# Performance work log

Measured on AMD Instinct MI355X. Metric: run time of the kernel, lower is better.

Reference implementation:

```python
import jax, jax.numpy as jnp
import numpy as np


def setup_inputs() -> dict:
    key = jax.random.key(0)
    ks = jax.random.split(key, 8)
    B, H, W, C = 4, 64, 64, 64
    Cf = C // 8
    x = jax.random.normal(ks[0], (B, H, W, C), dtype=jnp.float32)
    # 1x1 conv kernels stored as [C_in, C_out] (kernel_size=1)
    w_f = jax.random.normal(ks[1], (C, Cf), dtype=jnp.float32) * 0.05
    b_f = jax.random.normal(ks[2], (Cf,), dtype=jnp.float32) * 0.05
    w_g = jax.random.normal(ks[3], (C, Cf), dtype=jnp.float32) * 0.05
    b_g = jax.random.normal(ks[4], (Cf,), dtype=jnp.float32) * 0.05
    w_h = jax.random.normal(ks[5], (C, C), dtype=jnp.float32) * 0.05
    b_h = jax.random.normal(ks[6], (C,), dtype=jnp.float32) * 0.05
    gamma = jax.random.normal(ks[7], (1,), dtype=jnp.float32) * 0.1
    return {"x": x, "w_f": w_f, "b_f": b_f, "w_g": w_g, "b_g": b_g,
            "w_h": w_h, "b_h": b_h, "gamma": gamma}


def reference(x, w_f, b_f, w_g, b_g, w_h, b_h, gamma):
    B, H, W, C = x.shape
    N = H * W
    xf = x.reshape(B, N, C)  # 1x1 conv == per-pixel linear
    f = xf @ w_f + b_f       # [B, N, C/8]
    g = xf @ w_g + b_g       # [B, N, C/8]
    h = xf @ w_h + b_h       # [B, N, C]
    # attention_map[b, i, j] = <g_i, f_j>, softmax over last axis
    scores = jnp.einsum('bic,bjc->bij', g, f)  # [B, N, N]
    attn = jax.nn.softmax(scores, axis=-1)
    out = jnp.einsum('bij,bjc->bic', attn, h)  # [B, N, C]
    out = out.reshape(B, H, W, C)
    return gamma * out + x
```

## Files before the change

### kernel.cpp

```cpp
#include <hip/hip_runtime.h>
#include <hip/hip_bf16.h>

typedef __bf16 bf16;
typedef __bf16 bf16x8 __attribute__((ext_vector_type(8)));
typedef __bf16 bf16x4 __attribute__((ext_vector_type(4)));
typedef float floatx4 __attribute__((ext_vector_type(4)));

typedef int  aint  __attribute__((may_alias));
typedef long along __attribute__((may_alias));

#define NPIX 4096
#define BATCH 4
#define LOG2E 1.4426950408889634f
#define HT_BATCH 262144

__device__ inline bf16x8 zero8() {
    bf16x8 v;
    #pragma unroll
    for (int i = 0; i < 8; ++i) v[i] = (bf16)0.0f;
    return v;
}

__global__ __launch_bounds__(256) void proj_kernel(
    const float* __restrict__ x,
    const float* __restrict__ w_f, const float* __restrict__ b_f,
    const float* __restrict__ w_g, const float* __restrict__ b_g,
    const float* __restrict__ w_h, const float* __restrict__ b_h,
    bf16* __restrict__ fq, bf16* __restrict__ gq, unsigned char* __restrict__ hT)
{
    __shared__ bf16 xs[64 * 72];
    __shared__ bf16 wt[80 * 72];
    __shared__ float bs[80];
    const int tid = threadIdx.x;
    const int p0 = blockIdx.x * 64;

    {
        const float4* xg = (const float4*)(x + (long)p0 * 64);
        #pragma unroll
        for (int it = 0; it < 4; ++it) {
            int i4 = tid + it * 256;
            float4 v = xg[i4];
            int row = i4 >> 4, c4 = (i4 & 15) * 4;
            bf16x4 pk;
            pk[0] = (bf16)v.x; pk[1] = (bf16)v.y; pk[2] = (bf16)v.z; pk[3] = (bf16)v.w;
            *(bf16x4*)(&xs[row * 72 + c4]) = pk;
        }
    }
    for (int idx = tid; idx < 512; idx += 256) {
        int c = idx >> 3, n = idx & 7;
        wt[n * 72 + c]       = (bf16)w_f[idx];
        wt[(8 + n) * 72 + c] = (bf16)w_g[idx];
    }
    #pragma unroll
    for (int it = 0; it < 16; ++it) {
        int idx = tid + it * 256;
        int c = idx >> 6, n = idx & 63;
        wt[(16 + n) * 72 + c] = (bf16)w_h[idx];
    }
    if (tid < 80)
        bs[tid] = (tid < 8) ? b_f[tid] : (tid < 16) ? b_g[tid - 8] : b_h[tid - 16];
    __syncthreads();

    const int wv = tid >> 6, lane = tid & 63;
    const int quad = lane >> 4, l15 = lane & 15;
    const int b = blockIdx.x >> 6;
    const int n0pix = (p0 & (NPIX - 1)) + wv * 16 + quad * 4;

    bf16x8 a0 = *(const bf16x8*)(&xs[(wv * 16 + l15) * 72 + quad * 8]);
    bf16x8 a1 = *(const bf16x8*)(&xs[(wv * 16 + l15) * 72 + 32 + quad * 8]);

    #pragma unroll
    for (int nt = 0; nt < 5; ++nt) {
        float bias = bs[nt * 16 + l15];
        floatx4 acc = {bias, bias, bias, bias};
        bf16x8 b0 = *(const bf16x8*)(&wt[(nt * 16 + l15) * 72 + quad * 8]);
        bf16x8 b1 = *(const bf16x8*)(&wt[(nt * 16 + l15) * 72 + 32 + quad * 8]);
        acc = __builtin_amdgcn_mfma_f32_16x16x32_bf16(a0, b0, acc, 0, 0, 0);
        acc = __builtin_amdgcn_mfma_f32_16x16x32_bf16(a1, b1, acc, 0, 0, 0);
        if (nt == 0) {
            #pragma unroll
            for (int r = 0; r < 4; ++r) {
                long P = (long)p0 + wv * 16 + quad * 4 + r;
                if (l15 < 8) fq[P * 8 + l15] = (bf16)acc[r];
                else         gq[P * 8 + (l15 - 8)] = (bf16)(acc[r] * LOG2E);
            }
        } else {
            int c = nt * 16 + l15 - 16;
            int pk = __builtin_amdgcn_cvt_pk_fp8_f32(acc[0], acc[1], 0, false);
            pk     = __builtin_amdgcn_cvt_pk_fp8_f32(acc[2], acc[3], pk, true);
            *(aint*)(hT + (long)b * HT_BATCH + (n0pix >> 5) * 2048
                     + c * 32 + (n0pix & 31)) = pk;
        }
    }
}

__global__ __launch_bounds__(256, 4) void attn_kernel(
    const bf16* __restrict__ fq, const bf16* __restrict__ gq,
    const unsigned char* __restrict__ hT, const float* __restrict__ x,
    const float* __restrict__ gamma_p, float* __restrict__ out)
{
    __shared__ float red[4 * 32 * 68];
    const int tid  = threadIdx.x;
    const int wv   = tid >> 6, lane = tid & 63;
    const int quad = lane >> 4, l15 = lane & 15;
    const int jq   = wv;
    const int xcd = blockIdx.x & 7;
    const int b   = xcd >> 1;
    const int it  = ((blockIdx.x >> 3) & 63) | ((xcd & 1) << 6);
    const long rowbase = (long)b * NPIX + it * 32;
    const int jbase = jq * 1024;

    bf16x8 gfragA = zero8(), gfragB = zero8();
    if (lane < 16) {
        gfragA = *(const bf16x8*)(gq + (rowbase + lane) * 8);
        gfragB = *(const bf16x8*)(gq + (rowbase + 16 + lane) * 8);
    }

    const bf16* Fb = fq + ((long)b * NPIX + jbase) * 8;
    const unsigned char* Hb = hT + (long)b * HT_BATCH + (jbase >> 5) * 2048
                            + (l15 * 32 + quad * 8);

    floatx4 acc[8];
    #pragma unroll
    for (int k = 0; k < 8; ++k) acc[k] = (floatx4){0.f, 0.f, 0.f, 0.f};
    float denA = 0.f, denB = 0.f;

    const int idx_lo = (((quad & 1) * 2) * 16 + l15) * 4;
    const int idx_hi = idx_lo + 64;
    const bool sel_b = (quad >> 1) != 0;

    for (int t = 0; t < 8; ++t) {
        bf16x8 af[8];
        #pragma unroll
        for (int j8 = 0; j8 < 8; ++j8) {
            af[j8] = zero8();
            if (lane < 16)
                af[j8] = *(const bf16x8*)(Fb + (t * 128 + j8 * 16 + l15) * 8);
        }
        along bfr[16];
        #pragma unroll
        for (int ks = 0; ks < 4; ++ks)
            #pragma unroll
            for (int nt = 0; nt < 4; ++nt)
                bfr[ks * 4 + nt] = *(const along*)(Hb + (t * 4 + ks) * 2048 + nt * 512);

        int pkA[8], pkB[8];
        #pragma unroll
        for (int j8 = 0; j8 < 8; ++j8) {
            floatx4 sA = __builtin_amdgcn_mfma_f32_16x16x32_bf16(
                af[j8], gfragA, (floatx4){0.f, 0.f, 0.f, 0.f}, 0, 0, 0);
            floatx4 sB = __builtin_amdgcn_mfma_f32_16x16x32_bf16(
                af[j8], gfragB, (floatx4){0.f, 0.f, 0.f, 0.f}, 0, 0, 0);
            float a0 = __builtin_amdgcn_exp2f(sA[0]);
            float a1 = __builtin_amdgcn_exp2f(sA[1]);
            float a2 = __builtin_amdgcn_exp2f(sA[2]);
            float a3 = __builtin_amdgcn_exp2f(sA[3]);
            float b0 = __builtin_amdgcn_exp2f(sB[0]);
            float b1 = __builtin_amdgcn_exp2f(sB[1]);
            float b2 = __builtin_amdgcn_exp2f(sB[2]);
            float b3 = __builtin_amdgcn_exp2f(sB[3]);
            denA += (a0 + a1) + (a2 + a3);
            denB += (b0 + b1) + (b2 + b3);
            int pa = __builtin_amdgcn_cvt_pk_fp8_f32(a0, a1, 0, false);
            pkA[j8] = __builtin_amdgcn_cvt_pk_fp8_f32(a2, a3, pa, true);
            int pb = __builtin_amdgcn_cvt_pk_fp8_f32(b0, b1, 0, false);
            pkB[j8] = __builtin_amdgcn_cvt_pk_fp8_f32(b2, b3, pb, true);
        }
        #pragma unroll
        for (int ks = 0; ks < 4; ++ks) {
            int loA0 = __builtin_amdgcn_ds_bpermute(idx_lo, pkA[2 * ks]);
            int loA1 = __builtin_amdgcn_ds_bpermute(idx_lo, pkA[2 * ks + 1]);
            int hiA0 = __builtin_amdgcn_ds_bpermute(idx_hi, pkA[2 * ks]);
            int hiA1 = __builtin_amdgcn_ds_bpermute(idx_hi, pkA[2 * ks + 1]);
            unsigned loA = (unsigned)(sel_b ? loA1 : loA0);
            unsigned hiA = (unsigned)(sel_b ? hiA1 : hiA0);
            along pfA = (along)(((unsigned long)hiA << 32) | loA);
            int loB0 = __builtin_amdgcn_ds_bpermute(idx_lo, pkB[2 * ks]);
            int loB1 = __builtin_amdgcn_ds_bpermute(idx_lo, pkB[2 * ks + 1]);
            int hiB0 = __builtin_amdgcn_ds_bpermute(idx_hi, pkB[2 * ks]);
            int hiB1 = __builtin_amdgcn_ds_bpermute(idx_hi, pkB[2 * ks + 1]);
            unsigned loB = (unsigned)(sel_b ? loB1 : loB0);
            unsigned hiB = (unsigned)(sel_b ? hiB1 : hiB0);
            along pfB = (along)(((unsigned long)hiB << 32) | loB);
            #pragma unroll
            for (int nt = 0; nt < 4; ++nt) {
                acc[nt]     = __builtin_amdgcn_mfma_f32_16x16x32_fp8_fp8(
                    pfA, bfr[ks * 4 + nt], acc[nt], 0, 0, 0);
                acc[4 + nt] = __builtin_amdgcn_mfma_f32_16x16x32_fp8_fp8(
                    pfB, bfr[ks * 4 + nt], acc[4 + nt], 0, 0, 0);
            }
        }
    }

    denA += __shfl_xor(denA, 16);  denA += __shfl_xor(denA, 32);
    denB += __shfl_xor(denB, 16);  denB += __shfl_xor(denB, 32);

    {
        const int rbA = (jq * 32 + quad * 4) * 68;
        const int rbB = (jq * 32 + 16 + quad * 4) * 68;
        #pragma unroll
        for (int nt = 0; nt < 4; ++nt)
            #pragma unroll
            for (int r = 0; r < 4; ++r) {
                red[rbA + r * 68 + nt * 16 + l15] = acc[nt][r];
                red[rbB + r * 68 + nt * 16 + l15] = acc[4 + nt][r];
            }
        if (quad == 0) {
            red[(jq * 32 + l15) * 68 + 64]      = denA;
            red[(jq * 32 + 16 + l15) * 68 + 64] = denB;
        }
    }
    __syncthreads();

    {
        const int row = tid >> 3, c0 = (tid & 7) * 8;
        float4 n0 = {0.f, 0.f, 0.f, 0.f}, n1 = {0.f, 0.f, 0.f, 0.f};
        float den = 0.f;
        #pragma unroll
        for (int q = 0; q < 4; ++q) {
            const float* rr = red + (q * 32 + row) * 68;
            float4 a = *(const float4*)(rr + c0);
            float4 c = *(const float4*)(rr + c0 + 4);
            n0.x += a.x; n0.y += a.y; n0.z += a.z; n0.w += a.w;
            n1.x += c.x; n1.y += c.y; n1.z += c.z; n1.w += c.w;
            den += rr[64];
        }
        const float rd = gamma_p[0] / den;
        const long off = (rowbase + row) * 64 + c0;
        float4 xa = *(const float4*)(x + off);
        float4 xb = *(const float4*)(x + off + 4);
        float4 oa, ob;
        oa.x = n0.x * rd + xa.x; oa.y = n0.y * rd + xa.y;
        oa.z = n0.z * rd + xa.z; oa.w = n0.w * rd + xa.w;
        ob.x = n1.x * rd + xb.x; ob.y = n1.y * rd + xb.y;
        ob.z = n1.z * rd + xb.z; ob.w = n1.w * rd + xb.w;
        *(float4*)(out + off) = oa;
        *(float4*)(out + off + 4) = ob;
    }
}

extern "C" void kernel_launch(void* const* d_in, const int* in_sizes, int n_in,
                              void* d_out, int out_size, void* d_ws, size_t ws_size,
                              hipStream_t stream) {
    const float* x     = (const float*)d_in[0];
    const float* w_f   = (const float*)d_in[1];
    const float* b_f   = (const float*)d_in[2];
    const float* w_g   = (const float*)d_in[3];
    const float* b_g   = (const float*)d_in[4];
    const float* w_h   = (const float*)d_in[5];
    const float* b_h   = (const float*)d_in[6];
    const float* gamma = (const float*)d_in[7];
    float* out = (float*)d_out;

    bf16* fq = (bf16*)d_ws;
    bf16* gq = fq + 16384 * 8;
    unsigned char* hT = (unsigned char*)(gq + 16384 * 8);

    proj_kernel<<<256, 256, 0, stream>>>(x, w_f, b_f, w_g, b_g, w_h, b_h, fq, gq, hT);
    attn_kernel<<<512, 256, 0, stream>>>(fq, gq, hT, x, gamma, out);
}
```

Before: 95.57 us.

## Split key range across eight waves and use bit-trick exp2 approximation

Doubles the attention block to 512 threads so eight waves each handle 512 keys instead of four waves handling 1024. The final reduction now sums eight partials, with one float4 per thread. Separately, the hardware exp2 is replaced by a Schraudolph-style bit-trick approximation: an FMA followed by an int cast reinterpreted as float. This lowers transcendental cost, but the result is only piecewise-linear accurate, which relies on the later fp8 quantisation hiding the error. The doubled LDS reduction buffer and larger block may limit occupancy.

```diff
diff --git a/kernel.cpp b/kernel.cpp
--- a/kernel.cpp
+++ b/kernel.cpp
@@ -19,6 +19,11 @@
     #pragma unroll
     for (int i = 0; i < 8; ++i) v[i] = (bf16)0.0f;
     return v;
+}
+
+__device__ inline float fexp2a(float s) {
+    float y = __builtin_fmaf(s, 8388608.0f, 1064986823.0f);
+    return __int_as_float((int)y);
 }
 
 __global__ __launch_bounds__(256) void proj_kernel(
@@ -94,12 +99,12 @@
     }
 }
 
-__global__ __launch_bounds__(256, 4) void attn_kernel(
+__global__ __launch_bounds__(512, 4) void attn_kernel(
     const bf16* __restrict__ fq, const bf16* __restrict__ gq,
     const unsigned char* __restrict__ hT, const float* __restrict__ x,
     const float* __restrict__ gamma_p, float* __restrict__ out)
 {
-    __shared__ float red[4 * 32 * 68];
+    __shared__ float red[8 * 32 * 68];
     const int tid  = threadIdx.x;
     const int wv   = tid >> 6, lane = tid & 63;
     const int quad = lane >> 4, l15 = lane & 15;
@@ -108,7 +113,7 @@
     const int b   = xcd >> 1;
     const int it  = ((blockIdx.x >> 3) & 63) | ((xcd & 1) << 6);
     const long rowbase = (long)b * NPIX + it * 32;
-    const int jbase = jq * 1024;
+    const int jbase = jq * 512;
 
     bf16x8 gfragA = zero8(), gfragB = zero8();
     if (lane < 16) {
@@ -129,7 +134,7 @@
     const int idx_hi = idx_lo + 64;
     const bool sel_b = (quad >> 1) != 0;
 
-    for (int t = 0; t < 8; ++t) {
+    for (int t = 0; t < 4; ++t) {
         bf16x8 af[8];
         #pragma unroll
         for (int j8 = 0; j8 < 8; ++j8) {
@@ -151,14 +156,10 @@
                 af[j8], gfragA, (floatx4){0.f, 0.f, 0.f, 0.f}, 0, 0, 0);
             floatx4 sB = __builtin_amdgcn_mfma_f32_16x16x32_bf16(
                 af[j8], gfragB, (floatx4){0.f, 0.f, 0.f, 0.f}, 0, 0, 0);
-            float a0 = __builtin_amdgcn_exp2f(sA[0]);
-            float a1 = __builtin_amdgcn_exp2f(sA[1]);
-            float a2 = __builtin_amdgcn_exp2f(sA[2]);
-            float a3 = __builtin_amdgcn_exp2f(sA[3]);
-            float b0 = __builtin_amdgcn_exp2f(sB[0]);
-            float b1 = __builtin_amdgcn_exp2f(sB[1]);
-            float b2 = __builtin_amdgcn_exp2f(sB[2]);
-            float b3 = __builtin_amdgcn_exp2f(sB[3]);
+            float a0 = fexp2a(sA[0]), a1 = fexp2a(sA[1]);
+            float a2 = fexp2a(sA[2]), a3 = fexp2a(sA[3]);
+            float b0 = fexp2a(sB[0]), b1 = fexp2a(sB[1]);
+            float b2 = fexp2a(sB[2]), b3 = fexp2a(sB[3]);
             denA += (a0 + a1) + (a2 + a3);
             denB += (b0 + b1) + (b2 + b3);
             int pa = __builtin_amdgcn_cvt_pk_fp8_f32(a0, a1, 0, false);
@@ -213,29 +214,23 @@
     __syncthreads();
 
     {
-        const int row = tid >> 3, c0 = (tid & 7) * 8;
-        float4 n0 = {0.f, 0.f, 0.f, 0.f}, n1 = {0.f, 0.f, 0.f, 0.f};
+        const int row = tid >> 4, c0 = (tid & 15) * 4;
+        float4 n = {0.f, 0.f, 0.f, 0.f};
         float den = 0.f;
         #pragma unroll
-        for (int q = 0; q < 4; ++q) {
+        for (int q = 0; q < 8; ++q) {
             const float* rr = red + (q * 32 + row) * 68;
-            float4 a = *(const float4*)(rr + c0);
-            float4 c = *(const float4*)(rr + c0 + 4);
-            n0.x += a.x; n0.y += a.y; n0.z += a.z; n0.w += a.w;
-            n1.x += c.x; n1.y += c.y; n1.z += c.z; n1.w += c.w;
+            float4 v = *(const float4*)(rr + c0);
+            n.x += v.x; n.y += v.y; n.z += v.z; n.w += v.w;
             den += rr[64];
         }
         const float rd = gamma_p[0] / den;
         const long off = (rowbase + row) * 64 + c0;
-        float4 xa = *(const float4*)(x + off);
-        float4 xb = *(const float4*)(x + off + 4);
-        float4 oa, ob;
-        oa.x = n0.x * rd + xa.x; oa.y = n0.y * rd + xa.y;
-        oa.z = n0.z * rd + xa.z; oa.w = n0.w * rd + xa.w;
-        ob.x = n1.x * rd + xb.x; ob.y = n1.y * rd + xb.y;
-        ob.z = n1.z * rd + xb.z; ob.w = n1.w * rd + xb.w;
-        *(float4*)(out + off) = oa;
-        *(float4*)(out + off + 4) = ob;
+        float4 xv = *(const float4*)(x + off);
+        float4 o;
+        o.x = n.x * rd + xv.x; o.y = n.y * rd + xv.y;
+        o.z = n.z * rd + xv.z; o.w = n.w * rd + xv.w;
+        *(float4*)(out + off) = o;
     }
 }
 
@@ -257,5 +252,5 @@
     unsigned char* hT = (unsigned char*)(gq + 16384 * 8);
 
     proj_kernel<<<256, 256, 0, stream>>>(x, w_f, b_f, w_g, b_g, w_h, b_h, fq, gq, hT);
-    attn_kernel<<<512, 256, 0, stream>>>(fq, gq, hT, x, gamma, out);
-}
+    attn_kernel<<<512, 512, 0, stream>>>(fq, gq, hT, x, gamma, out);
+}
```

Measured after the change: 127.2 us. +33.1%, slower.
